# Optimization experiments

Hardware: AMD Instinct MI355X
Metric: run time of the kernel (lower is better)

Reference implementation:

```python
import jax, jax.numpy as jnp
import numpy as np

B, T, I, H, O = 2048, 512, 6, 50, 3


def setup_inputs() -> dict:
    key = jax.random.key(0)
    ks = jax.random.split(key, 7)
    s = 1.0 / np.sqrt(H).astype(np.float32)
    u = lambda k, shape: jax.random.uniform(k, shape, jnp.float32, -s, s)
    return {
        "x": jax.random.normal(ks[0], (B, T, I), jnp.float32),
        # PyTorch nn.LSTM params, gate order [i, f, g, o] stacked on dim 0
        "W_ih": u(ks[1], (4 * H, I)),
        "W_hh": u(ks[2], (4 * H, H)),
        "b_ih": u(ks[3], (4 * H,)),
        "b_hh": u(ks[4], (4 * H,)),
        # Linear(50, 3)
        "W_out": u(ks[5], (O, H)),
        "b_out": u(ks[6], (O,)),
    }


def reference(x, W_ih, W_hh, b_ih, b_hh, W_out, b_out):
    b = x.shape[0]
    h0 = jnp.zeros((b, H), x.dtype)
    c0 = jnp.zeros((b, H), x.dtype)
    bias = b_ih + b_hh  # [4H]

    def step(carry, x_t):
        h, c = carry
        # gates: [B, 4H], PyTorch order i, f, g, o
        g = x_t @ W_ih.T + h @ W_hh.T + bias
        i, f, gg, o = jnp.split(g, 4, axis=-1)
        c = jax.nn.sigmoid(f) * c + jax.nn.sigmoid(i) * jnp.tanh(gg)
        h = jax.nn.sigmoid(o) * jnp.tanh(c)
        return (h, c), None

    # scan over time; only the final hidden state is needed (x[:, -1, :])
    (h_last, _), _ = jax.lax.scan(step, (h0, c0), jnp.swapaxes(x, 0, 1))
    logits = h_last @ W_out.T + b_out  # [B, 3]
    return jax.nn.softmax(logits, axis=1)
```

## Files before the change

### kernel.cpp

```cpp
#include <hip/hip_runtime.h>


#define L2E 1.44269504088896340736f

typedef float  f32x4  __attribute__((ext_vector_type(4)));
typedef short  s16x8  __attribute__((ext_vector_type(8)));

__device__ __forceinline__ float fast_exp2(float x){ return __builtin_amdgcn_exp2f(x); }
__device__ __forceinline__ float fast_rcp (float x){ return __builtin_amdgcn_rcpf(x); }
__device__ __forceinline__ float sigm_p(float y){ return fast_rcp(1.0f + fast_exp2(-y)); }
__device__ __forceinline__ float tanh_p(float y){ return 1.0f - 2.0f * fast_rcp(1.0f + fast_exp2(y)); }

__device__ __forceinline__ unsigned short f2bf(float f){
  unsigned u = __builtin_bit_cast(unsigned, f);
  u = (u + 0x7FFFu + ((u >> 16) & 1u)) >> 16;
  return (unsigned short)u;
}

constexpr int B_ = 2048, T_ = 512, I_ = 6, H_ = 50;
constexpr int NB = 8;
constexpr int AP = 72;
constexpr int T6 = T_ * I_;

__global__ __launch_bounds__(512, 1)
void lstm_kernel(const float* __restrict__ x,
                 const float* __restrict__ W_ih, const float* __restrict__ W_hh,
                 const float* __restrict__ b_ih, const float* __restrict__ b_hh,
                 const float* __restrict__ W_out, const float* __restrict__ b_out,
                 float* __restrict__ out)
{
  __shared__ unsigned short Xpack[T_][NB][8];
  __shared__ unsigned short Abuf[2][16 * AP];
  __shared__ float Hlast[NB][H_];

  const int tid  = threadIdx.x;
  const int lane = tid & 63;
  const int wave = tid >> 6;
  const int col  = lane & 15;
  const int quad = lane >> 4;
  const int b0   = blockIdx.x * NB;

  #pragma unroll
  for (int i = 0; i < NB; i++) {
    const float* xp = x + (size_t)(b0 + i) * T6 + tid * I_;
    const float2 a0 = *(const float2*)(xp);
    const float2 a1 = *(const float2*)(xp + 2);
    const float2 a2 = *(const float2*)(xp + 4);
    unsigned* dst = (unsigned*)&Xpack[tid][i][0];
    dst[0] = (unsigned)f2bf(a0.x) | ((unsigned)f2bf(a0.y) << 16);
    dst[1] = (unsigned)f2bf(a1.x) | ((unsigned)f2bf(a1.y) << 16);
    dst[2] = (unsigned)f2bf(a2.x) | ((unsigned)f2bf(a2.y) << 16);
    dst[3] = 0x3F80u;
  }

  for (int i = tid; i < 2 * 16 * AP; i += 512) (&Abuf[0][0])[i] = 0;

  const int ntw = (wave < 5) ? 2 : 1;
  s16x8 wf[2][2];
  #pragma unroll
  for (int ti = 0; ti < 2; ti++) {
    if (ti < ntw) {
      const int jp = (wave + 8 * ti) * 16 + col;
      const bool ok = jp < 200;
      const int hidx = jp >> 2, g = jp & 3;
      const int row = g * 50 + hidx;
      const float scl = (g == 2) ? (2.0f * L2E) : L2E;
      #pragma unroll
      for (int kh = 0; kh < 2; kh++) {
        s16x8 w;
        #pragma unroll
        for (int kk = 0; kk < 8; kk++) {
          const int k = kh * 32 + quad * 8 + kk;
          float v = 0.0f;
          if (ok) {
            if      (k < 48)  v = W_hh[row * 50 + k];
            else if (k < 54)  v = W_ih[row * 6 + (k - 48)];
            else if (k == 54) v = b_ih[row] + b_hh[row];
            else if (k == 56) v = W_hh[row * 50 + 48];
            else if (k == 57) v = W_hh[row * 50 + 49];
          }
          w[kk] = (short)f2bf(v * scl);
        }
        wf[ti][kh] = w;
      }
    }
  }

  const int ti_r  = col >> 3;
  const int b_r   = col & 7;
  const int jt_r  = wave + 8 * ti_r;
  const int hh    = 4 * jt_r + quad;
  const bool valid = (jt_r < 13) && (hh < H_);
  const int pos   = hh + ((hh >= 48) ? 8 : 0);

  float c_ = 0.0f, hreg = 0.0f;

  __syncthreads();

  #pragma unroll 2
  for (int t = 0; t < T_; t++) {
    const unsigned short* Ar = &Abuf[t & 1][0];
    unsigned short*       Aw = &Abuf[(t + 1) & 1][0];

    const unsigned short* arow = Ar + col * AP;
    const s16x8 bfr0 = *(const s16x8*)(arow + quad * 8);
    const unsigned short* p1 = (quad == 2) ? &Xpack[t][b_r][0]
                                           : (arow + 32 + quad * 8);
    const s16x8 bfr1 = *(const s16x8*)p1;

    f32x4 a0 = {0.f, 0.f, 0.f, 0.f};
    a0 = __builtin_amdgcn_mfma_f32_16x16x32_bf16(wf[0][0], bfr0, a0, 0, 0, 0);
    a0 = __builtin_amdgcn_mfma_f32_16x16x32_bf16(wf[0][1], bfr1, a0, 0, 0, 0);
    f32x4 g = a0;
    if (wave < 5) {
      f32x4 a1 = {0.f, 0.f, 0.f, 0.f};
      a1 = __builtin_amdgcn_mfma_f32_16x16x32_bf16(wf[1][0], bfr0, a1, 0, 0, 0);
      a1 = __builtin_amdgcn_mfma_f32_16x16x32_bf16(wf[1][1], bfr1, a1, 0, 0, 0);
      #pragma unroll
      for (int r = 0; r < 4; r++) {
        const float o = __shfl_xor(a1[r], 8, 64);
        g[r] = (ti_r == 0) ? a0[r] : o;
      }
    }

    if (valid) {
      const float gi = sigm_p(g[0]);
      const float gf = sigm_p(g[1]);
      const float gg = tanh_p(g[2]);
      const float go = sigm_p(g[3]);
      c_ = gf * c_ + gi * gg;
      hreg = go * tanh_p(c_ * (2.0f * L2E));
      Aw[b_r * AP + pos] = f2bf(hreg);
    }

    __syncthreads();
  }

  if (valid) Hlast[b_r][hh] = hreg;
  __syncthreads();

  if (tid < NB) {
    float l[3];
    #pragma unroll
    for (int o = 0; o < 3; o++) {
      float s = b_out[o];
      for (int k = 0; k < H_; k++) s += W_out[o * H_ + k] * Hlast[tid][k];
      l[o] = s;
    }
    const float m  = fmaxf(l[0], fmaxf(l[1], l[2]));
    const float e0 = fast_exp2((l[0] - m) * L2E);
    const float e1 = fast_exp2((l[1] - m) * L2E);
    const float e2 = fast_exp2((l[2] - m) * L2E);
    const float inv = fast_rcp(e0 + e1 + e2);
    float* op = out + (size_t)(b0 + tid) * 3;
    op[0] = e0 * inv; op[1] = e1 * inv; op[2] = e2 * inv;
  }
}

extern "C" void kernel_launch(void* const* d_in, const int* in_sizes, int n_in,
                              void* d_out, int out_size, void* d_ws, size_t ws_size,
                              hipStream_t stream) {
  const float* x     = (const float*)d_in[0];
  const float* W_ih  = (const float*)d_in[1];
  const float* W_hh  = (const float*)d_in[2];
  const float* b_ih  = (const float*)d_in[3];
  const float* b_hh  = (const float*)d_in[4];
  const float* W_out = (const float*)d_in[5];
  const float* b_out = (const float*)d_in[6];
  lstm_kernel<<<B_ / NB, 512, 0, stream>>>(x, W_ih, W_hh, b_ih, b_hh,
                                           W_out, b_out, (float*)d_out);
}
```

Before: 242.7 us.

## Use 4 waves per block with hoisted input-projection MFMA and fused gate math

Halves the block to 256 threads (4 waves), with each wave computing four 16-row gate tiles and two hidden cells per lane, which cuts the barrier participants per timestep. The x·W_ih+bias contribution moves into a separate MFMA computed one step ahead and used as the accumulator seed, so the recurrent MFMAs only read h from shared memory. The gate nonlinearities are fused to share reciprocals, with clamping for stability. The trade-off is more MFMAs and more serial activation work per wave on the critical path, and fewer waves to hide latency.

```diff
diff --git a/kernel.cpp b/kernel.cpp
--- a/kernel.cpp
+++ b/kernel.cpp
@@ -3,13 +3,11 @@
 
 #define L2E 1.44269504088896340736f
 
-typedef float  f32x4  __attribute__((ext_vector_type(4)));
-typedef short  s16x8  __attribute__((ext_vector_type(8)));
+typedef float  f32x4 __attribute__((ext_vector_type(4)));
+typedef short  s16x8 __attribute__((ext_vector_type(8)));
 
 __device__ __forceinline__ float fast_exp2(float x){ return __builtin_amdgcn_exp2f(x); }
 __device__ __forceinline__ float fast_rcp (float x){ return __builtin_amdgcn_rcpf(x); }
-__device__ __forceinline__ float sigm_p(float y){ return fast_rcp(1.0f + fast_exp2(-y)); }
-__device__ __forceinline__ float tanh_p(float y){ return 1.0f - 2.0f * fast_rcp(1.0f + fast_exp2(y)); }
 
 __device__ __forceinline__ unsigned short f2bf(float f){
   unsigned u = __builtin_bit_cast(unsigned, f);
@@ -17,12 +15,27 @@
   return (unsigned short)u;
 }
 
+__device__ __forceinline__ float lstm_cell(const f32x4 g, float& c){
+  const float ef = fast_exp2(-g[1]);
+  const float sf = fast_rcp(1.0f + ef);
+  const float yg = fminf(fmaxf(g[2], -115.f), 115.f);
+  const float eg = fast_exp2(yg);
+  const float ei = fast_exp2(-g[0]);
+  const float r1 = fast_rcp((1.0f + ei) * (1.0f + eg));
+  c = sf * c + (eg - 1.0f) * r1;
+  const float yc = fminf(fmaxf(c * (2.0f * L2E), -115.f), 115.f);
+  const float ec = fast_exp2(yc);
+  const float eo = fast_exp2(-g[3]);
+  const float r2 = fast_rcp((1.0f + eo) * (1.0f + ec));
+  return (ec - 1.0f) * r2;
+}
+
 constexpr int B_ = 2048, T_ = 512, I_ = 6, H_ = 50;
 constexpr int NB = 8;
 constexpr int AP = 72;
 constexpr int T6 = T_ * I_;
 
-__global__ __launch_bounds__(512, 1)
+__global__ __launch_bounds__(256, 1)
 void lstm_kernel(const float* __restrict__ x,
                  const float* __restrict__ W_ih, const float* __restrict__ W_hh,
                  const float* __restrict__ b_ih, const float* __restrict__ b_hh,
@@ -30,7 +43,7 @@
                  float* __restrict__ out)
 {
   __shared__ unsigned short Xpack[T_][NB][8];
-  __shared__ unsigned short Abuf[2][16 * AP];
+  __shared__ unsigned short Abuf[2][NB * AP];
   __shared__ float Hlast[NB][H_];
 
   const int tid  = threadIdx.x;
@@ -38,105 +51,116 @@
   const int wave = tid >> 6;
   const int col  = lane & 15;
   const int quad = lane >> 4;
+  const int bb   = col & 7;
+  const bool lo  = col < 8;
   const int b0   = blockIdx.x * NB;
 
+  for (int tt = tid; tt < T_; tt += 256) {
+    #pragma unroll
+    for (int i = 0; i < NB; i++) {
+      const float* xp = x + (size_t)(b0 + i) * T6 + tt * I_;
+      const float2 a0 = *(const float2*)(xp);
+      const float2 a1 = *(const float2*)(xp + 2);
+      const float2 a2 = *(const float2*)(xp + 4);
+      unsigned* dst = (unsigned*)&Xpack[tt][i][0];
+      dst[0] = (unsigned)f2bf(a0.x) | ((unsigned)f2bf(a0.y) << 16);
+      dst[1] = (unsigned)f2bf(a1.x) | ((unsigned)f2bf(a1.y) << 16);
+      dst[2] = (unsigned)f2bf(a2.x) | ((unsigned)f2bf(a2.y) << 16);
+      dst[3] = 0x3F80u;
+    }
+  }
+  for (int i = tid; i < 2 * NB * AP; i += 256) (&Abuf[0][0])[i] = 0;
+
+  s16x8 wfh[4][2], wfx[4];
   #pragma unroll
-  for (int i = 0; i < NB; i++) {
-    const float* xp = x + (size_t)(b0 + i) * T6 + tid * I_;
-    const float2 a0 = *(const float2*)(xp);
-    const float2 a1 = *(const float2*)(xp + 2);
-    const float2 a2 = *(const float2*)(xp + 4);
-    unsigned* dst = (unsigned*)&Xpack[tid][i][0];
-    dst[0] = (unsigned)f2bf(a0.x) | ((unsigned)f2bf(a0.y) << 16);
-    dst[1] = (unsigned)f2bf(a1.x) | ((unsigned)f2bf(a1.y) << 16);
-    dst[2] = (unsigned)f2bf(a2.x) | ((unsigned)f2bf(a2.y) << 16);
-    dst[3] = 0x3F80u;
+  for (int ti = 0; ti < 4; ti++) {
+    const int jp = (wave + 4 * ti) * 16 + col;
+    const bool ok = jp < 200;
+    const int hidx = jp >> 2, gat = jp & 3;
+    const int row = gat * 50 + hidx;
+    const float scl = (gat == 2) ? (2.0f * L2E) : L2E;
+    #pragma unroll
+    for (int kh = 0; kh < 2; kh++) {
+      s16x8 w;
+      #pragma unroll
+      for (int kk = 0; kk < 8; kk++) {
+        const int k = kh * 32 + quad * 8 + kk;
+        const float v = (ok && k < 50) ? W_hh[row * 50 + k] : 0.0f;
+        w[kk] = (short)f2bf(v * scl);
+      }
+      wfh[ti][kh] = w;
+    }
+    s16x8 wx;
+    #pragma unroll
+    for (int kk = 0; kk < 8; kk++) {
+      float v = 0.0f;
+      if (ok && quad == 0) {
+        if      (kk < 6)  v = W_ih[row * 6 + kk];
+        else if (kk == 6) v = b_ih[row] + b_hh[row];
+      }
+      wx[kk] = (short)f2bf(v * scl);
+    }
+    wfx[ti] = wx;
   }
 
-  for (int i = tid; i < 2 * 16 * AP; i += 512) (&Abuf[0][0])[i] = 0;
+  const int hh0 = 4 * (wave + 4 * (lo ? 0 : 1)) + quad;
+  const int hh1 = hh0 + 32;
+  const bool valid1 = lo || (wave == 0 && quad < 2);
 
-  const int ntw = (wave < 5) ? 2 : 1;
-  s16x8 wf[2][2];
-  #pragma unroll
-  for (int ti = 0; ti < 2; ti++) {
-    if (ti < ntw) {
-      const int jp = (wave + 8 * ti) * 16 + col;
-      const bool ok = jp < 200;
-      const int hidx = jp >> 2, g = jp & 3;
-      const int row = g * 50 + hidx;
-      const float scl = (g == 2) ? (2.0f * L2E) : L2E;
-      #pragma unroll
-      for (int kh = 0; kh < 2; kh++) {
-        s16x8 w;
-        #pragma unroll
-        for (int kk = 0; kk < 8; kk++) {
-          const int k = kh * 32 + quad * 8 + kk;
-          float v = 0.0f;
-          if (ok) {
-            if      (k < 48)  v = W_hh[row * 50 + k];
-            else if (k < 54)  v = W_ih[row * 6 + (k - 48)];
-            else if (k == 54) v = b_ih[row] + b_hh[row];
-            else if (k == 56) v = W_hh[row * 50 + 48];
-            else if (k == 57) v = W_hh[row * 50 + 49];
-          }
-          w[kk] = (short)f2bf(v * scl);
-        }
-        wf[ti][kh] = w;
-      }
-    }
-  }
-
-  const int ti_r  = col >> 3;
-  const int b_r   = col & 7;
-  const int jt_r  = wave + 8 * ti_r;
-  const int hh    = 4 * jt_r + quad;
-  const bool valid = (jt_r < 13) && (hh < H_);
-  const int pos   = hh + ((hh >= 48) ? 8 : 0);
-
-  float c_ = 0.0f, hreg = 0.0f;
+  float c0 = 0.f, c1 = 0.f, h0r = 0.f, h1r = 0.f;
+  const f32x4 zz = {0.f, 0.f, 0.f, 0.f};
 
   __syncthreads();
+
+  f32x4 accx[4];
+  {
+    const s16x8 bx = *(const s16x8*)&Xpack[0][bb][0];
+    #pragma unroll
+    for (int ti = 0; ti < 4; ti++)
+      accx[ti] = __builtin_amdgcn_mfma_f32_16x16x32_bf16(wfx[ti], bx, zz, 0, 0, 0);
+  }
 
   #pragma unroll 2
   for (int t = 0; t < T_; t++) {
     const unsigned short* Ar = &Abuf[t & 1][0];
     unsigned short*       Aw = &Abuf[(t + 1) & 1][0];
 
-    const unsigned short* arow = Ar + col * AP;
+    const unsigned short* arow = Ar + bb * AP;
     const s16x8 bfr0 = *(const s16x8*)(arow + quad * 8);
-    const unsigned short* p1 = (quad == 2) ? &Xpack[t][b_r][0]
-                                           : (arow + 32 + quad * 8);
-    const s16x8 bfr1 = *(const s16x8*)p1;
+    const s16x8 bfr1 = *(const s16x8*)(arow + 32 + quad * 8);
 
-    f32x4 a0 = {0.f, 0.f, 0.f, 0.f};
-    a0 = __builtin_amdgcn_mfma_f32_16x16x32_bf16(wf[0][0], bfr0, a0, 0, 0, 0);
-    a0 = __builtin_amdgcn_mfma_f32_16x16x32_bf16(wf[0][1], bfr1, a0, 0, 0, 0);
-    f32x4 g = a0;
-    if (wave < 5) {
-      f32x4 a1 = {0.f, 0.f, 0.f, 0.f};
-      a1 = __builtin_amdgcn_mfma_f32_16x16x32_bf16(wf[1][0], bfr0, a1, 0, 0, 0);
-      a1 = __builtin_amdgcn_mfma_f32_16x16x32_bf16(wf[1][1], bfr1, a1, 0, 0, 0);
-      #pragma unroll
-      for (int r = 0; r < 4; r++) {
-        const float o = __shfl_xor(a1[r], 8, 64);
-        g[r] = (ti_r == 0) ? a0[r] : o;
-      }
+    f32x4 a[4];
+    #pragma unroll
+    for (int ti = 0; ti < 4; ti++) {
+      a[ti] = __builtin_amdgcn_mfma_f32_16x16x32_bf16(wfh[ti][0], bfr0, accx[ti], 0, 0, 0);
+      a[ti] = __builtin_amdgcn_mfma_f32_16x16x32_bf16(wfh[ti][1], bfr1, a[ti],    0, 0, 0);
     }
 
-    if (valid) {
-      const float gi = sigm_p(g[0]);
-      const float gf = sigm_p(g[1]);
-      const float gg = tanh_p(g[2]);
-      const float go = sigm_p(g[3]);
-      c_ = gf * c_ + gi * gg;
-      hreg = go * tanh_p(c_ * (2.0f * L2E));
-      Aw[b_r * AP + pos] = f2bf(hreg);
+    {
+      const s16x8 bx = *(const s16x8*)&Xpack[(t + 1) & (T_ - 1)][bb][0];
+      #pragma unroll
+      for (int ti = 0; ti < 4; ti++)
+        accx[ti] = __builtin_amdgcn_mfma_f32_16x16x32_bf16(wfx[ti], bx, zz, 0, 0, 0);
     }
+
+    f32x4 g0, g1;
+    #pragma unroll
+    for (int r = 0; r < 4; r++) {
+      g0[r] = lo ? a[0][r] : a[1][r];
+      g1[r] = lo ? a[2][r] : a[3][r];
+    }
+
+    h0r = lstm_cell(g0, c0);
+    h1r = lstm_cell(g1, c1);
+
+    Aw[bb * AP + hh0] = f2bf(h0r);
+    if (valid1) Aw[bb * AP + hh1] = f2bf(h1r);
 
     __syncthreads();
   }
 
-  if (valid) Hlast[b_r][hh] = hreg;
+  Hlast[bb][hh0] = h0r;
+  if (valid1) Hlast[bb][hh1] = h1r;
   __syncthreads();
 
   if (tid < NB) {
@@ -167,6 +191,6 @@
   const float* b_hh  = (const float*)d_in[4];
   const float* W_out = (const float*)d_in[5];
   const float* b_out = (const float*)d_in[6];
-  lstm_kernel<<<B_ / NB, 512, 0, stream>>>(x, W_ih, W_hh, b_ih, b_hh,
+  lstm_kernel<<<B_ / NB, 256, 0, stream>>>(x, W_ih, W_hh, b_ih, b_hh,
                                            W_out, b_out, (float*)d_out);
 }
```

Measured after the change: 259.4 us. +6.9%, slower.
